# Optimization experiments

Hardware: AMD Instinct MI355X
Metric: run time of the kernel (lower is better)

Reference implementation:

```python
import jax, jax.numpy as jnp
import numpy as np

N = 256          # args.image_size
B = 64           # args.batch_size
K = 5            # args.kernel_size
RHO = 1
ETA = 1.0
IDEN_OFF = 4.0   # identity_offset
DEF_OFF = (2.0 + IDEN_OFF / (N - 1)) / 2.0   # deforming_offset
SCALE = IDEN_OFF / (N - 1)


def _iden_grid():
    # torch.arange(-(N-1), N, 2) / (N-1): N values from -1 to 1
    seq = jnp.arange(-(N - 1), N, 2) / (N - 1.0)
    gx = jnp.broadcast_to(seq[None, :], (N, N))   # x varies along width
    return jnp.stack([gx, gx.T], 0)[None]          # [1,2,N,N]


def _gauss2d():
    sigma = K * 0.15 + 0.35
    half = (K - 1) * 0.5
    x = jnp.linspace(-half, half, K)
    pdf = jnp.exp(-0.5 * (x / sigma) ** 2)
    k1 = pdf / pdf.sum()
    return jnp.outer(k1, k1)                        # [K,K]


def _forward(image, prim_grid):
    Bsz = prim_grid.shape[0]
    # --- gaussian_blur: reflect pad + depthwise conv ---
    pad = K // 2
    pg = jnp.pad(prim_grid, ((0, 0), (0, 0), (pad, pad), (pad, pad)), mode='reflect')
    kern = jnp.broadcast_to(_gauss2d(), (2, 1, K, K))
    pg = jax.lax.conv_general_dilated(
        pg, kern, (1, 1), 'VALID',
        dimension_numbers=('NCHW', 'OIHW', 'NCHW'), feature_group_count=2)
    iden = _iden_grid()
    # --- prim -> samp, samp -> accu (the [1,-1] conv_transpose == shifted diff) ---
    s = pg + iden + DEF_OFF                           # [B,2,N,N]
    sx, sy = s[:, 0], s[:, 1]
    zx = jnp.zeros((Bsz, N, 1), sx.dtype)
    zy = jnp.zeros((Bsz, 1, N), sy.dtype)
    accu_x = (sx - jnp.concatenate([zx, sx[:, :, :-1]], axis=2)) / SCALE
    accu_y = (sy - jnp.concatenate([zy, sy[:, :-1, :]], axis=1)) / SCALE
    # --- accu_clip ---
    accu_x = jax.nn.relu(accu_x)
    accu_y = jax.nn.relu(accu_y)
    # --- accu -> samp (all-ones-kernel conv_transpose == cumsum) ---
    samp_x = jnp.cumsum(accu_x * SCALE, axis=2) - DEF_OFF
    samp_y = jnp.cumsum(accu_y * SCALE, axis=1) - DEF_OFF
    samp = jnp.stack([samp_x, samp_y], 1)             # [B,2,N,N]
    # --- prim_clip then samp_clip ---
    pw = 2.0 / N
    prim = jnp.clip(samp - iden, -pw * RHO, pw * RHO)
    samp = jnp.clip(prim + iden, -ETA, ETA)
    # --- grid_sample: bilinear, align_corners=True, zeros padding ---
    gx, gy = samp[:, 0], samp[:, 1]                   # [B,N,N]
    Himg, Wimg = image.shape[2], image.shape[3]
    ix = (gx + 1.0) * 0.5 * (Wimg - 1)
    iy = (gy + 1.0) * 0.5 * (Himg - 1)
    x0 = jnp.floor(ix)
    y0 = jnp.floor(iy)
    wx1 = ix - x0
    wy1 = iy - y0
    b = jnp.arange(Bsz)[:, None, None]

    def corner(xc, yc):
        valid = ((xc >= 0) & (xc <= Wimg - 1) & (yc >= 0) & (yc <= Himg - 1)).astype(image.dtype)
        xi = jnp.clip(xc, 0, Wimg - 1).astype(jnp.int32)
        yi = jnp.clip(yc, 0, Himg - 1).astype(jnp.int32)
        return image[b, :, yi, xi] * valid[..., None]   # [B,N,N,C]

    out = (corner(x0, y0) * ((1 - wx1) * (1 - wy1))[..., None]
           + corner(x0 + 1, y0) * (wx1 * (1 - wy1))[..., None]
           + corner(x0, y0 + 1) * ((1 - wx1) * wy1)[..., None]
           + corner(x0 + 1, y0 + 1) * (wx1 * wy1)[..., None])
    return jnp.transpose(out, (0, 3, 1, 2))            # [B,C,N,N]


def setup_inputs() -> dict:
    key = jax.random.key(0)
    k1, k2 = jax.random.split(key)
    image = jax.random.normal(k1, (B, 3, N, N), dtype=jnp.float32)
    prim_grid = jax.random.normal(k2, (B, 2, N, N), dtype=jnp.float32)
    return {"image": image, "prim_grid": prim_grid}


def reference(image, prim_grid):
    return _forward(image, prim_grid)
```

## Files before the change

### kernel.cpp

```cpp
#include <hip/hip_runtime.h>

namespace {

constexpr int Nn = 256;
constexpr int Bn = 64;
constexpr int SEG = 8;
constexpr int NSEG = Nn / SEG;

constexpr float KW0 = 0.07076638f;
constexpr float KW1 = 0.24446039f;
constexpr float KW2 = 0.36954646f;

constexpr float DEF_OFF   = 1.00784313725490196f;
constexpr float SCALE     = 0.01568627450980392f;
constexpr float INV_SCALE = 63.75f;
constexpr float TWO255    = 0.00784313725490196f;
constexpr float PW        = 0.0078125f;

__device__ __forceinline__ int reflN(int i) {
    if (i < 0) i = -i;
    if (i >= Nn) i = 2 * (Nn - 1) - i;
    return i;
}

__device__ __forceinline__ float seqf(int t) {
    return (float)(2 * t - (Nn - 1)) * (1.0f / (float)(Nn - 1));
}

__device__ __forceinline__ void segb(int lin, int& seg, int& b) {
    int wg = (lin & 7) * 256 + (lin >> 3);
    b = wg >> 5;
    seg = wg & (NSEG - 1);
}

__global__ __launch_bounds__(256, 8) void kP_kernel(const float* __restrict__ prim,
                                                    float* __restrict__ partial) {
    const int j = threadIdx.x;
    int seg, b;
    segb(blockIdx.x, seg, b);
    const int i0 = seg * SEG;
    const float* c1 = prim + ((size_t)b * 2 + 1) * Nn * Nn;

    float a[SEG + 5];
    #pragma unroll
    for (int t = 0; t < SEG + 5; ++t) a[t] = c1[reflN(i0 - 3 + t) * Nn + j];

    __shared__ float vb[(SEG + 1) * Nn];
    #pragma unroll
    for (int r = 0; r < SEG + 1; ++r)
        vb[r * Nn + j] = KW0 * (a[r] + a[r + 4]) + KW1 * (a[r + 1] + a[r + 3]) + KW2 * a[r + 2];
    __syncthreads();

    const int jm2 = reflN(j - 2), jm1 = reflN(j - 1), jp1 = reflN(j + 1), jp2 = reflN(j + 2);
    auto hc = [&](const float* v) {
        return KW0 * (v[jm2] + v[jp2]) + KW1 * (v[jm1] + v[jp1]) + KW2 * v[j];
    };

    float hprev = hc(&vb[0]);
    float psum = 0.0f;
    #pragma unroll
    for (int r = 0; r < SEG; ++r) {
        float h = hc(&vb[(r + 1) * Nn]);
        float hm = (r == 0 && seg == 0) ? 0.0f : hprev;
        psum += fmaxf((h - hm + TWO255) * INV_SCALE, 0.0f);
        hprev = h;
    }
    partial[((size_t)b * NSEG + seg) * Nn + j] = psum;
}

__global__ __launch_bounds__(256, 4) void kF_kernel(const float* __restrict__ prim,
                                                    const float* __restrict__ image,
                                                    const float* __restrict__ partial,
                                                    float* __restrict__ outp) {
    const int j = threadIdx.x;
    int seg, b;
    segb(blockIdx.x, seg, b);
    const int i0 = seg * SEG;
    const int lane = j & 63;
    const int wave = j >> 6;

    __shared__ float imgT[3][SEG + 2][Nn];
    __shared__ float vb[(SEG + 1) * Nn];
    __shared__ float wsum[SEG][4];

    for (int t = wave; t < 3 * (SEG + 2); t += 4) {
        int c = t / (SEG + 2), r = t % (SEG + 2);
        int row = min(max(i0 - 1 + r, 0), Nn - 1);
        const float* src = image + ((size_t)(b * 3 + c) * Nn + row) * Nn + lane * 4;
#if defined(__has_builtin) && __has_builtin(__builtin_amdgcn_global_load_lds)
        __builtin_amdgcn_global_load_lds(
            (const __attribute__((address_space(1))) void*)(const void*)src,
            (__attribute__((address_space(3))) void*)(void*)&imgT[c][r][0],
            16, 0, 0);
#else
        ((float4*)&imgT[c][r][0])[lane] = ((const float4*)(src - lane * 4))[lane];
#endif
    }

    const float* c0 = prim + (size_t)b * 2 * Nn * Nn;
    const float* c1 = c0 + (size_t)Nn * Nn;

    const float* pb = partial + (size_t)b * NSEG * Nn + j;
    float carry = 0.0f;
    #pragma unroll
    for (int k = 0; k < NSEG - 1; ++k) {
        float p = pb[(size_t)k * Nn];
        carry += (k < seg) ? p : 0.0f;
    }

    const int jm3 = reflN(j - 3), jm2 = reflN(j - 2), jm1 = reflN(j - 1),
              jp1 = reflN(j + 1), jp2 = reflN(j + 2);
    auto hc = [&](const float* v) {
        return KW0 * (v[jm2] + v[jp2]) + KW1 * (v[jm1] + v[jp1]) + KW2 * v[j];
    };

    float accu[SEG];
    {
        float a[SEG + 5];
        #pragma unroll
        for (int t = 0; t < SEG + 5; ++t) a[t] = c1[reflN(i0 - 3 + t) * Nn + j];
        #pragma unroll
        for (int r = 0; r < SEG + 1; ++r)
            vb[r * Nn + j] = KW0 * (a[r] + a[r + 4]) + KW1 * (a[r + 1] + a[r + 3]) + KW2 * a[r + 2];
        __syncthreads();
        float hprev = hc(&vb[0]);
        #pragma unroll
        for (int r = 0; r < SEG; ++r) {
            float h = hc(&vb[(r + 1) * Nn]);
            float hm = (r == 0 && seg == 0) ? 0.0f : hprev;
            accu[r] = fmaxf((h - hm + TWO255) * INV_SCALE, 0.0f);
            hprev = h;
        }
        __syncthreads();
    }

    float ix[SEG];
    {
        float a[SEG + 4];
        #pragma unroll
        for (int t = 0; t < SEG + 4; ++t) a[t] = c0[reflN(i0 - 2 + t) * Nn + j];
        #pragma unroll
        for (int r = 0; r < SEG; ++r)
            vb[r * Nn + j] = KW0 * (a[r] + a[r + 4]) + KW1 * (a[r + 1] + a[r + 3]) + KW2 * a[r + 2];
        __syncthreads();
        #pragma unroll
        for (int r = 0; r < SEG; ++r) {
            const float* v = &vb[r * Nn];
            float h  = hc(v);
            float hm = KW0 * (v[jm3] + v[jp1]) + KW1 * (v[jm2] + v[j]) + KW2 * v[jm1];
            if (j == 0) hm = 0.0f;
            float s = fmaxf((h - hm + TWO255) * INV_SCALE, 0.0f);
            #pragma unroll
            for (int off = 1; off < 64; off <<= 1) {
                float u = __shfl_up(s, off, 64);
                if (lane >= off) s += u;
            }
            ix[r] = s;
            if (lane == 63) wsum[r][wave] = s;
        }
        __syncthreads();
        const float sq_j = seqf(j);
        #pragma unroll
        for (int r = 0; r < SEG; ++r) {
            float add = 0.0f;
            for (int w = 0; w < wave; ++w) add += wsum[r][w];
            float samp = (ix[r] + add) * SCALE - DEF_OFF;
            float p = fminf(fmaxf(samp - sq_j, -PW), PW);
            float g = fminf(fmaxf(p + sq_j, -1.0f), 1.0f);
            ix[r] = (g + 1.0f) * 127.5f;
        }
    }

    float iy[SEG];
    {
        float cum = carry;
        #pragma unroll
        for (int k = 0; k < SEG; ++k) {
            cum += accu[k];
            float samp = cum * SCALE - DEF_OFF;
            float sq = seqf(i0 + k);
            float p  = fminf(fmaxf(samp - sq, -PW), PW);
            float gy = fminf(fmaxf(p + sq, -1.0f), 1.0f);
            iy[k] = (gy + 1.0f) * 127.5f;
        }
    }

    #pragma unroll
    for (int c = 0; c < 3; ++c) {
        const float (*tile)[Nn] = imgT[c];
        #pragma unroll
        for (int k = 0; k < SEG; ++k) {
            float fx = floorf(ix[k]), fy = floorf(iy[k]);
            int x0 = (int)fx, y0 = (int)fy;
            float wx1 = ix[k] - fx, wy1 = iy[k] - fy;
            float wx0 = 1.0f - wx1, wy0 = 1.0f - wy1;
            bool vx1 = x0 < Nn - 1, vy1 = y0 < Nn - 1;
            int x1c = min(x0 + 1, Nn - 1);
            int ly0 = y0 - i0 + 1;
            int ly1 = min(y0 + 1, Nn - 1) - i0 + 1;
            float w00 = wx0 * wy0;
            float w10 = vx1 ? wx1 * wy0 : 0.0f;
            float w01 = vy1 ? wx0 * wy1 : 0.0f;
            float w11 = (vx1 && vy1) ? wx1 * wy1 : 0.0f;
            float v = w00 * tile[ly0][x0] + w10 * tile[ly0][x1c]
                    + w01 * tile[ly1][x0] + w11 * tile[ly1][x1c];
            __builtin_nontemporal_store(v, &outp[(((size_t)b * 3 + c) * Nn + (i0 + k)) * Nn + j]);
        }
    }
}

}

extern "C" void kernel_launch(void* const* d_in, const int* in_sizes, int n_in,
                              void* d_out, int out_size, void* d_ws, size_t ws_size,
                              hipStream_t stream) {
    const float* image = (const float*)d_in[0];
    const float* prim  = (const float*)d_in[1];
    float* outp = (float*)d_out;
    float* partial = (float*)d_ws;

    kP_kernel<<<NSEG * Bn, 256, 0, stream>>>(prim, partial);
    kF_kernel<<<NSEG * Bn, 256, 0, stream>>>(prim, image, partial, outp);
}
```

Measured before the change: 38.42 us.

## Double-buffer image channel tiles in LDS to raise kF occupancy

Replaces the three per-channel image tiles plus a separate blur scratch buffer with two shared buffers. Channel tiles are now streamed through them: channel 0 is prefetched into one buffer while the blur runs, and channels 1 and 2 are loaded while earlier channels are being interpolated. Bilinear weights and indices are computed once and reused for all three channels, and launch bounds go from 4 to 7 blocks. The smaller LDS footprint is meant to allow more resident blocks and to overlap image loads with compute. The cost is extra barriers, serialised channel loads, and more registers held for the precomputed weights.

```diff
diff --git a/kernel.cpp b/kernel.cpp
--- a/kernel.cpp
+++ b/kernel.cpp
@@ -68,7 +68,7 @@
     partial[((size_t)b * NSEG + seg) * Nn + j] = psum;
 }
 
-__global__ __launch_bounds__(256, 4) void kF_kernel(const float* __restrict__ prim,
+__global__ __launch_bounds__(256, 7) void kF_kernel(const float* __restrict__ prim,
                                                     const float* __restrict__ image,
                                                     const float* __restrict__ partial,
                                                     float* __restrict__ outp) {
@@ -79,23 +79,26 @@
     const int lane = j & 63;
     const int wave = j >> 6;
 
-    __shared__ float imgT[3][SEG + 2][Nn];
-    __shared__ float vb[(SEG + 1) * Nn];
+    __shared__ float bufA[SEG + 2][Nn];
+    __shared__ float bufB[SEG + 2][Nn];
     __shared__ float wsum[SEG][4];
 
-    for (int t = wave; t < 3 * (SEG + 2); t += 4) {
-        int c = t / (SEG + 2), r = t % (SEG + 2);
-        int row = min(max(i0 - 1 + r, 0), Nn - 1);
-        const float* src = image + ((size_t)(b * 3 + c) * Nn + row) * Nn + lane * 4;
+    auto issue_prefetch = [&](int c, float (*buf)[Nn]) {
+        for (int r = wave; r < SEG + 2; r += 4) {
+            int row = min(max(i0 - 1 + r, 0), Nn - 1);
+            const float* src = image + ((size_t)(b * 3 + c) * Nn + row) * Nn + lane * 4;
 #if defined(__has_builtin) && __has_builtin(__builtin_amdgcn_global_load_lds)
-        __builtin_amdgcn_global_load_lds(
-            (const __attribute__((address_space(1))) void*)(const void*)src,
-            (__attribute__((address_space(3))) void*)(void*)&imgT[c][r][0],
-            16, 0, 0);
+            __builtin_amdgcn_global_load_lds(
+                (const __attribute__((address_space(1))) void*)(const void*)src,
+                (__attribute__((address_space(3))) void*)(void*)&buf[r][0],
+                16, 0, 0);
 #else
-        ((float4*)&imgT[c][r][0])[lane] = ((const float4*)(src - lane * 4))[lane];
+            ((float4*)&buf[r][0])[lane] = ((const float4*)(src - lane * 4))[lane];
 #endif
-    }
+        }
+    };
+
+    issue_prefetch(0, bufA);
 
     const float* c0 = prim + (size_t)b * 2 * Nn * Nn;
     const float* c1 = c0 + (size_t)Nn * Nn;
@@ -121,12 +124,12 @@
         for (int t = 0; t < SEG + 5; ++t) a[t] = c1[reflN(i0 - 3 + t) * Nn + j];
         #pragma unroll
         for (int r = 0; r < SEG + 1; ++r)
-            vb[r * Nn + j] = KW0 * (a[r] + a[r + 4]) + KW1 * (a[r + 1] + a[r + 3]) + KW2 * a[r + 2];
-        __syncthreads();
-        float hprev = hc(&vb[0]);
+            bufB[r][j] = KW0 * (a[r] + a[r + 4]) + KW1 * (a[r + 1] + a[r + 3]) + KW2 * a[r + 2];
+        __syncthreads();
+        float hprev = hc(&bufB[0][0]);
         #pragma unroll
         for (int r = 0; r < SEG; ++r) {
-            float h = hc(&vb[(r + 1) * Nn]);
+            float h = hc(&bufB[r + 1][0]);
             float hm = (r == 0 && seg == 0) ? 0.0f : hprev;
             accu[r] = fmaxf((h - hm + TWO255) * INV_SCALE, 0.0f);
             hprev = h;
@@ -141,11 +144,11 @@
         for (int t = 0; t < SEG + 4; ++t) a[t] = c0[reflN(i0 - 2 + t) * Nn + j];
         #pragma unroll
         for (int r = 0; r < SEG; ++r)
-            vb[r * Nn + j] = KW0 * (a[r] + a[r + 4]) + KW1 * (a[r + 1] + a[r + 3]) + KW2 * a[r + 2];
+            bufB[r][j] = KW0 * (a[r] + a[r + 4]) + KW1 * (a[r + 1] + a[r + 3]) + KW2 * a[r + 2];
         __syncthreads();
         #pragma unroll
         for (int r = 0; r < SEG; ++r) {
-            const float* v = &vb[r * Nn];
+            const float* v = &bufB[r][0];
             float h  = hc(v);
             float hm = KW0 * (v[jm3] + v[jp1]) + KW1 * (v[jm2] + v[j]) + KW2 * v[jm1];
             if (j == 0) hm = 0.0f;
@@ -159,6 +162,11 @@
             if (lane == 63) wsum[r][wave] = s;
         }
         __syncthreads();
+    }
+
+    issue_prefetch(1, bufB);
+
+    {
         const float sq_j = seqf(j);
         #pragma unroll
         for (int r = 0; r < SEG; ++r) {
@@ -185,28 +193,40 @@
         }
     }
 
-    #pragma unroll
-    for (int c = 0; c < 3; ++c) {
-        const float (*tile)[Nn] = imgT[c];
+    float w00[SEG], w10[SEG], w01[SEG], w11[SEG];
+    int xx0[SEG], xx1[SEG], yy0[SEG], yy1[SEG];
+    #pragma unroll
+    for (int k = 0; k < SEG; ++k) {
+        float fx = floorf(ix[k]), fy = floorf(iy[k]);
+        int x0 = (int)fx, y0 = (int)fy;
+        float wx1 = ix[k] - fx, wy1 = iy[k] - fy;
+        float wx0 = 1.0f - wx1, wy0 = 1.0f - wy1;
+        bool vx1 = x0 < Nn - 1, vy1 = y0 < Nn - 1;
+        xx0[k] = x0;
+        xx1[k] = min(x0 + 1, Nn - 1);
+        yy0[k] = y0 - i0 + 1;
+        yy1[k] = min(y0 + 1, Nn - 1) - i0 + 1;
+        w00[k] = wx0 * wy0;
+        w10[k] = vx1 ? wx1 * wy0 : 0.0f;
+        w01[k] = vy1 ? wx0 * wy1 : 0.0f;
+        w11[k] = (vx1 && vy1) ? wx1 * wy1 : 0.0f;
+    }
+
+    auto interp_store = [&](int c, const float (*tile)[Nn]) {
         #pragma unroll
         for (int k = 0; k < SEG; ++k) {
-            float fx = floorf(ix[k]), fy = floorf(iy[k]);
-            int x0 = (int)fx, y0 = (int)fy;
-            float wx1 = ix[k] - fx, wy1 = iy[k] - fy;
-            float wx0 = 1.0f - wx1, wy0 = 1.0f - wy1;
-            bool vx1 = x0 < Nn - 1, vy1 = y0 < Nn - 1;
-            int x1c = min(x0 + 1, Nn - 1);
-            int ly0 = y0 - i0 + 1;
-            int ly1 = min(y0 + 1, Nn - 1) - i0 + 1;
-            float w00 = wx0 * wy0;
-            float w10 = vx1 ? wx1 * wy0 : 0.0f;
-            float w01 = vy1 ? wx0 * wy1 : 0.0f;
-            float w11 = (vx1 && vy1) ? wx1 * wy1 : 0.0f;
-            float v = w00 * tile[ly0][x0] + w10 * tile[ly0][x1c]
-                    + w01 * tile[ly1][x0] + w11 * tile[ly1][x1c];
+            float v = w00[k] * tile[yy0[k]][xx0[k]] + w10[k] * tile[yy0[k]][xx1[k]]
+                    + w01[k] * tile[yy1[k]][xx0[k]] + w11[k] * tile[yy1[k]][xx1[k]];
             __builtin_nontemporal_store(v, &outp[(((size_t)b * 3 + c) * Nn + (i0 + k)) * Nn + j]);
         }
-    }
+    };
+
+    interp_store(0, bufA);
+    __syncthreads();
+    issue_prefetch(2, bufA);
+    interp_store(1, bufB);
+    __syncthreads();
+    interp_store(2, bufA);
 }
 
 }
```

Measured after the change: 85.01 us. +121.3%, slower.
